# Performance work log

Hardware: AMD Instinct MI355X
Metric: run time of the kernel (lower is better)

## Reference

```python
import jax, jax.numpy as jnp
import numpy as np

B, S, HID = 2, 2048, 1024
NH, HD = 16, 64
EPS = 1e-12


def setup_inputs() -> dict:
    key = jax.random.key(0)
    ks = jax.random.split(key, 6)
    w_scale = 1.0 / np.sqrt(HID)
    return {
        "hidden_states": jax.random.normal(ks[0], (B, S, HID), dtype=jnp.float32),
        "attention_mask": jnp.ones((B, S), dtype=jnp.float32),
        "Wq": jax.random.normal(ks[1], (HID, HID), dtype=jnp.float32) * w_scale,
        "bq": jnp.zeros((HID,), dtype=jnp.float32),
        "Wk": jax.random.normal(ks[2], (HID, HID), dtype=jnp.float32) * w_scale,
        "bk": jnp.zeros((HID,), dtype=jnp.float32),
        "Wv": jax.random.normal(ks[3], (HID, HID), dtype=jnp.float32) * w_scale,
        "bv": jnp.zeros((HID,), dtype=jnp.float32),
        "Wd": jax.random.normal(ks[4], (HID, HID), dtype=jnp.float32) * w_scale,
        "bd": jnp.zeros((HID,), dtype=jnp.float32),
        "ln_gamma": jnp.ones((HID,), dtype=jnp.float32),
        "ln_beta": jnp.zeros((HID,), dtype=jnp.float32),
    }


def _heads(x):  # [B,S,HID] -> [B,NH,S,HD]
    return x.reshape(B, S, NH, HD).transpose(0, 2, 1, 3)


def reference(hidden_states, attention_mask, Wq, bq, Wk, bk, Wv, bv, Wd, bd, ln_gamma, ln_beta):
    # pre-LayerNorm
    mu = jnp.mean(hidden_states, axis=-1, keepdims=True)
    var = jnp.mean(jnp.square(hidden_states - mu), axis=-1, keepdims=True)
    h = (hidden_states - mu) * jax.lax.rsqrt(var + EPS) * ln_gamma + ln_beta

    q = _heads(h @ Wq.T + bq)  # [B,NH,S,HD]
    k = _heads(h @ Wk.T + bk)
    v = _heads(h @ Wv.T + bv)

    # additive mask: -1000 * (1 - mask), broadcast over heads and query pos
    add_mask = -1000.0 * (1.0 - attention_mask)[:, None, None, :]  # [B,1,1,S]

    # scale applied symmetrically to q and k: sqrt(sqrt(HD)) each
    scale = np.sqrt(np.sqrt(HD)).astype(np.float32)
    scores = jnp.einsum("bhqd,bhkd->bhqk", q / scale, k / scale) + add_mask
    probs = jax.nn.softmax(scores, axis=-1)  # dropout p=0 -> identity
    ctx = jnp.einsum("bhqk,bhkd->bhqd", probs, v)  # [B,NH,S,HD]

    ctx = ctx.transpose(0, 2, 1, 3).reshape(B, S, HID)
    return ctx @ Wd.T + bd
```

## Files before the change

kernel.cpp:

```cpp
#include <hip/hip_runtime.h>
#include <math.h>

#define BATCH 2
#define SEQ   2048
#define HID   1024
#define NH    16
#define HD    64
#define MROWS (BATCH * SEQ)
#define VSTR  4160

typedef unsigned short u16;
typedef short bf16x8 __attribute__((ext_vector_type(8)));
typedef float f32x4  __attribute__((ext_vector_type(4)));

#define LOG2E 1.4426950408889634f
#define C2    (0.125f * LOG2E)
#define M2F   23.083120f

static __device__ __forceinline__ u16 f2bf(float f) {
    union { float f; unsigned int u; } v; v.f = f;
    unsigned int r = (v.u + 0x7FFF + ((v.u >> 16) & 1)) >> 16;
    return (u16)r;
}

static __device__ __forceinline__ f32x4 mfma16(bf16x8 a, bf16x8 b, f32x4 c) {
    return __builtin_amdgcn_mfma_f32_16x16x32_bf16(a, b, c, 0, 0, 0);
}

static __device__ __forceinline__ void ldsload16(const void* g, void* l) {
    __builtin_amdgcn_global_load_lds(
        (const __attribute__((address_space(1))) void*)(unsigned long long)(uintptr_t)g,
        (__attribute__((address_space(3))) void*)(unsigned int)(uintptr_t)l,
        16, 0, 0);
}

__global__ __launch_bounds__(256) void prep_kernel(const float* __restrict__ x,
                                                   const float* __restrict__ gamma,
                                                   const float* __restrict__ beta,
                                                   u16* __restrict__ h,
                                                   const float* __restrict__ w0,
                                                   const float* __restrict__ w1,
                                                   const float* __restrict__ w2,
                                                   const float* __restrict__ w3,
                                                   u16* o0, u16* o1, u16* o2, u16* o3)
{
    __shared__ float red[8];
    const int t = threadIdx.x;
    if (blockIdx.x < 4096) {
        const int blk = blockIdx.x;
        const int which = blk >> 10;
        const int lb = blk & 1023;
        const float* src = which == 0 ? w0 : which == 1 ? w1 : which == 2 ? w2 : w3;
        u16* dst = which == 0 ? o0 : which == 1 ? o1 : which == 2 ? o2 : o3;
        const int idx = (lb * 256 + t) * 4;
        const float4 f = *(const float4*)(src + idx);
        union { u16 s[4]; uint2 v; } p;
        p.s[0] = f2bf(f.x); p.s[1] = f2bf(f.y); p.s[2] = f2bf(f.z); p.s[3] = f2bf(f.w);
        *(uint2*)(dst + idx) = p.v;
        return;
    }
    const int row = blockIdx.x - 4096;
    const float4 xv = ((const float4*)(x + (size_t)row * HID))[t];
    float s  = xv.x + xv.y + xv.z + xv.w;
    float ss = xv.x * xv.x + xv.y * xv.y + xv.z * xv.z + xv.w * xv.w;
#pragma unroll
    for (int off = 32; off > 0; off >>= 1) {
        s  += __shfl_down(s, off);
        ss += __shfl_down(ss, off);
    }
    const int wid = t >> 6;
    if ((t & 63) == 0) { red[wid] = s; red[4 + wid] = ss; }
    __syncthreads();
    s  = red[0] + red[1] + red[2] + red[3];
    ss = red[4] + red[5] + red[6] + red[7];
    const float mu   = s * (1.0f / HID);
    const float var  = ss * (1.0f / HID) - mu * mu;
    const float rstd = rsqrtf(var + 1e-12f);
    const float4 g  = ((const float4*)gamma)[t];
    const float4 bb = ((const float4*)beta)[t];
    union { u16 s[4]; uint2 v; } p;
    p.s[0] = f2bf((xv.x - mu) * rstd * g.x + bb.x);
    p.s[1] = f2bf((xv.y - mu) * rstd * g.y + bb.y);
    p.s[2] = f2bf((xv.z - mu) * rstd * g.z + bb.z);
    p.s[3] = f2bf((xv.w - mu) * rstd * g.w + bb.w);
    ((uint2*)(h + (size_t)row * HID))[t] = p.v;
}

static __device__ __forceinline__ void gemm_core(const u16* __restrict__ A,
                                                 const u16* __restrict__ B,
                                                 int K, int bm, int bn,
                                                 u16* As, u16* Bs,
                                                 int wave, int lane,
                                                 f32x4 acc[4][4])
{
    const int l15  = lane & 15;
    const int quad = lane >> 4;
    const int wm = (wave >> 1) * 64;
    const int wn = (wave & 1) * 64;

    const int c1 = wave * 64 + lane;
    const int c2 = c1 + 256;
    const u16* A1 = A + (size_t)(bm + (c1 >> 2)) * K + (c1 & 3) * 8;
    const u16* A2 = A + (size_t)(bm + (c2 >> 2)) * K + (c2 & 3) * 8;
    const u16* B1 = B + (size_t)(bn + (c1 >> 2)) * K + (c1 & 3) * 8;
    const u16* B2 = B + (size_t)(bn + (c2 >> 2)) * K + (c2 & 3) * 8;
    u16* lA1 = As + wave * 512;
    u16* lA2 = As + 2048 + wave * 512;
    u16* lB1 = Bs + wave * 512;
    u16* lB2 = Bs + 2048 + wave * 512;

    for (int k0 = 0; k0 < K; k0 += 32) {
        __syncthreads();
        ldsload16(A1 + k0, lA1);
        ldsload16(A2 + k0, lA2);
        ldsload16(B1 + k0, lB1);
        ldsload16(B2 + k0, lB2);
        __syncthreads();
        bf16x8 af[4], bfr[4];
#pragma unroll
        for (int mt = 0; mt < 4; mt++)
            af[mt] = *(const bf16x8*)&As[(wm + mt * 16 + l15) * 32 + quad * 8];
#pragma unroll
        for (int nt = 0; nt < 4; nt++)
            bfr[nt] = *(const bf16x8*)&Bs[(wn + nt * 16 + l15) * 32 + quad * 8];
#pragma unroll
        for (int mt = 0; mt < 4; mt++)
#pragma unroll
            for (int nt = 0; nt < 4; nt++)
                acc[mt][nt] = mfma16(af[mt], bfr[nt], acc[mt][nt]);
    }
}

__global__ __launch_bounds__(256) void qkv_gemm(const u16* __restrict__ h,
                                                const u16* __restrict__ wq,
                                                const u16* __restrict__ wk,
                                                const u16* __restrict__ wv,
                                                const float* __restrict__ bq,
                                                const float* __restrict__ bk,
                                                const float* __restrict__ bv,
                                                u16* __restrict__ qo,
                                                u16* __restrict__ ko,
                                                u16* __restrict__ vo)
{
    __shared__ u16 As[4096];
    __shared__ u16 Bs[4096];
    const int blk  = blockIdx.x;
    const int wave = threadIdx.x >> 6;
    const int lane = threadIdx.x & 63;
    const int l15  = lane & 15;
    const int quad = lane >> 4;
    const int wm = (wave >> 1) * 64;
    const int wn = (wave & 1) * 64;

    f32x4 acc[4][4];
#pragma unroll
    for (int mt = 0; mt < 4; mt++)
#pragma unroll
        for (int nt = 0; nt < 4; nt++) acc[mt][nt] = (f32x4)0.0f;

    if (blk < 512) {
        const u16* W     = (blk < 256) ? wq : wk;
        const float* bia = (blk < 256) ? bq : bk;
        u16* out         = (blk < 256) ? qo : ko;
        const int local = blk & 255;
        const int bm = (local >> 3) * 128;
        const int bn = (local & 7) * 128;
        gemm_core(h, W, HID, bm, bn, As, Bs, wave, lane, acc);

        float bv4[4];
#pragma unroll
        for (int nt = 0; nt < 4; nt++) bv4[nt] = bia[bn + wn + nt * 16 + l15];
#pragma unroll
        for (int mt = 0; mt < 4; mt++)
#pragma unroll
            for (int r = 0; r < 4; r++) {
                const int m  = bm + wm + mt * 16 + quad * 4 + r;
                const int bI = m >> 11;
                const int sI = m & (SEQ - 1);
#pragma unroll
                for (int nt = 0; nt < 4; nt++) {
                    const int n  = bn + wn + nt * 16 + l15;
                    const int hh = n >> 6;
                    const int d  = n & 63;
                    out[(((size_t)(bI * NH + hh) * SEQ + sI) << 6) + d] =
                        f2bf(acc[mt][nt][r] + bv4[nt]);
                }
            }
    } else {
        const int local = blk - 512;
        const int bm = (local & 7) * 128;
        const int bn = (local >> 3) * 128;
        gemm_core(wv, h, HID, bm, bn, As, Bs, wave, lane, acc);

#pragma unroll
        for (int mt = 0; mt < 4; mt++) {
            const f32x4 bm4 = *(const f32x4*)&bv[bm + wm + mt * 16 + quad * 4];
#pragma unroll
            for (int r = 0; r < 4; r++) {
                const int row = bm + wm + mt * 16 + quad * 4 + r;
#pragma unroll
                for (int nt = 0; nt < 4; nt++) {
                    const int col = bn + wn + nt * 16 + l15;
                    vo[(size_t)row * VSTR + col] = f2bf(acc[mt][nt][r] + bm4[r]);
                }
            }
        }
    }
}

__global__ __launch_bounds__(256) void out_gemm(const u16* __restrict__ ctx,
                                                const u16* __restrict__ wd,
                                                const float* __restrict__ bd,
                                                float* __restrict__ out)
{
    __shared__ u16 As[4096];
    __shared__ u16 Bs[4096];
    const int blk  = blockIdx.x;
    const int wave = threadIdx.x >> 6;
    const int lane = threadIdx.x & 63;
    const int l15  = lane & 15;
    const int quad = lane >> 4;
    const int wm = (wave >> 1) * 64;
    const int wn = (wave & 1) * 64;
    const int bm = (blk >> 3) * 128;
    const int bn = (blk & 7) * 128;

    f32x4 acc[4][4];
#pragma unroll
    for (int mt = 0; mt < 4; mt++)
#pragma unroll
        for (int nt = 0; nt < 4; nt++) acc[mt][nt] = (f32x4)0.0f;

    gemm_core(ctx, wd, HID, bm, bn, As, Bs, wave, lane, acc);

    float bv4[4];
#pragma unroll
    for (int nt = 0; nt < 4; nt++) bv4[nt] = bd[bn + wn + nt * 16 + l15];
#pragma unroll
    for (int mt = 0; mt < 4; mt++)
#pragma unroll
        for (int r = 0; r < 4; r++) {
            const int m = bm + wm + mt * 16 + quad * 4 + r;
#pragma unroll
            for (int nt = 0; nt < 4; nt++) {
                const int n = bn + wn + nt * 16 + l15;
                out[(size_t)m * HID + n] = acc[mt][nt][r] + bv4[nt];
            }
        }
}

__global__ __launch_bounds__(256) void attn_mfma(const u16* __restrict__ qb,
                                                 const u16* __restrict__ kb,
                                                 const u16* __restrict__ vtb,
                                                 const float* __restrict__ maskg,
                                                 u16* __restrict__ ctx)
{
    __shared__ __align__(16) char smem[25856];
    u16* Ks  = (u16*)smem;
    u16* Vts = (u16*)(smem + 8192);
    u16 (*Pw)[72] = (u16(*)[72])(smem + 16384 + (threadIdx.x >> 6) * 2304);
    float* Ms2 = (float*)(smem + 25600);

    const int t    = threadIdx.x;
    const int wave = t >> 6;
    const int lane = t & 63;
    const int l15  = lane & 15;
    const int quad = lane >> 4;

    const int bh = blockIdx.x & 31;
    const int qt = blockIdx.x >> 5;
    const int b  = bh >> 4;
    const int hh = bh & 15;
    const int q0 = qt * 64;

    const size_t headoff = (size_t)(b * NH + hh) * SEQ * HD;
    const u16* kbase = kb + headoff;
    const u16* vbase = vtb + (size_t)(hh * HD) * VSTR + b * SEQ;

    bf16x8 Qf[2];
    {
        const int qrow = q0 + wave * 16 + l15;
#pragma unroll
        for (int ks = 0; ks < 2; ks++)
            Qf[ks] = *(const bf16x8*)(qb + headoff + (size_t)qrow * HD + ks * 32 + quad * 8);
    }

    f32x4 O[4];
#pragma unroll
    for (int mt = 0; mt < 4; mt++) O[mt] = (f32x4)0.0f;
    float lsum = 0.0f;

    const int srow = lane >> 3;
    const int lcol = (lane & 7) ^ srow;
    const int sw0 = ((quad)     ^ (l15 & 7)) * 8;
    const int sw1 = ((quad + 4) ^ (l15 & 7)) * 8;

    for (int c0 = 0; c0 < SEQ; c0 += 64) {
        __syncthreads();
        {
            const int g0 = wave * 2;
            ldsload16(kbase + (size_t)(c0 + g0 * 8 + srow) * HD + lcol * 8,
                      (char*)Ks + g0 * 1024);
            ldsload16(kbase + (size_t)(c0 + g0 * 8 + 8 + srow) * HD + lcol * 8,
                      (char*)Ks + g0 * 1024 + 1024);
            ldsload16(vbase + (size_t)(g0 * 8 + srow) * VSTR + c0 + lcol * 8,
                      (char*)Vts + g0 * 1024);
            ldsload16(vbase + (size_t)(g0 * 8 + 8 + srow) * VSTR + c0 + lcol * 8,
                      (char*)Vts + g0 * 1024 + 1024);
            if (t < 64)
                Ms2[t] = fmaf(-1000.0f * (1.0f - maskg[b * SEQ + c0 + t]), LOG2E, -M2F);
        }
        __syncthreads();

        f32x4 St[4];
#pragma unroll
        for (int mt = 0; mt < 4; mt++) {
            const int rb = (mt * 16 + l15) * 64;
            const bf16x8 ka0 = *(const bf16x8*)&Ks[rb + sw0];
            const bf16x8 ka1 = *(const bf16x8*)&Ks[rb + sw1];
            f32x4 a = (f32x4)0.0f;
            a = mfma16(ka0, Qf[0], a);
            a = mfma16(ka1, Qf[1], a);
            St[mt] = a;
        }

#pragma unroll
        for (int mt = 0; mt < 4; mt++) {
            const f32x4 mv = *(const f32x4*)&Ms2[mt * 16 + quad * 4];
            union { u16 s[4]; uint2 v; } pk;
#pragma unroll
            for (int r = 0; r < 4; r++) {
                const float p = __builtin_amdgcn_exp2f(fmaf(St[mt][r], C2, mv[r]));
                lsum += p;
                pk.s[r] = f2bf(p);
            }
            *(uint2*)&Pw[l15][mt * 16 + quad * 4] = pk.v;
        }

        const bf16x8 Pb0 = *(const bf16x8*)&Pw[l15][quad * 8];
        const bf16x8 Pb1 = *(const bf16x8*)&Pw[l15][32 + quad * 8];

#pragma unroll
        for (int mt = 0; mt < 4; mt++) {
            const int rb = (mt * 16 + l15) * 64;
            const bf16x8 va0 = *(const bf16x8*)&Vts[rb + sw0];
            const bf16x8 va1 = *(const bf16x8*)&Vts[rb + sw1];
            O[mt] = mfma16(va0, Pb0, O[mt]);
            O[mt] = mfma16(va1, Pb1, O[mt]);
        }
    }

    lsum += __shfl_xor(lsum, 16);
    lsum += __shfl_xor(lsum, 32);
    const float linv = 1.0f / lsum;

    __syncthreads();
    float* Ot = (float*)smem + wave * (16 * 68);
#pragma unroll
    for (int mt = 0; mt < 4; mt++) {
        f32x4 v = O[mt] * linv;
        *(f32x4*)(Ot + l15 * 68 + mt * 16 + quad * 4) = v;
    }
    __syncthreads();
    {
        const int ql  = lane >> 2;
        const int seg = lane & 3;
        const float* srcp = Ot + ql * 68 + seg * 16;
        u16* dstp = ctx + (size_t)(b * SEQ + q0 + wave * 16 + ql) * HID
                        + hh * 64 + seg * 16;
#pragma unroll
        for (int j = 0; j < 2; j++) {
            union { u16 s[8]; uint4 v; } p;
#pragma unroll
            for (int i = 0; i < 8; i++) p.s[i] = f2bf(srcp[j * 8 + i]);
            *(uint4*)(dstp + j * 8) = p.v;
        }
    }
}

extern "C" void kernel_launch(void* const* d_in, const int* in_sizes, int n_in,
                              void* d_out, int out_size, void* d_ws, size_t ws_size,
                              hipStream_t stream)
{
    const float* hs    = (const float*)d_in[0];
    const float* mask  = (const float*)d_in[1];
    const float* Wq    = (const float*)d_in[2];
    const float* bq    = (const float*)d_in[3];
    const float* Wk    = (const float*)d_in[4];
    const float* bk    = (const float*)d_in[5];
    const float* Wv    = (const float*)d_in[6];
    const float* bv    = (const float*)d_in[7];
    const float* Wd    = (const float*)d_in[8];
    const float* bd    = (const float*)d_in[9];
    const float* gamma = (const float*)d_in[10];
    const float* beta  = (const float*)d_in[11];
    float* out = (float*)d_out;

    const size_t NE = (size_t)MROWS * HID;
    u16* ws   = (u16*)d_ws;
    u16* h    = ws;
    u16* qbb  = ws + NE;
    u16* kbb  = qbb + NE;
    u16* vtb  = kbb + NE;
    u16* ctxb = vtb + (size_t)HID * VSTR;
    u16* wqb  = ctxb + NE;
    u16* wkb  = wqb + HID * HID;
    u16* wvb  = wkb + HID * HID;
    u16* wdb  = wvb + HID * HID;

    prep_kernel<<<8192, 256, 0, stream>>>(hs, gamma, beta, h,
                                          Wq, Wk, Wv, Wd, wqb, wkb, wvb, wdb);

    qkv_gemm<<<768, 256, 0, stream>>>(h, wqb, wkb, wvb, bq, bk, bv, qbb, kbb, vtb);

    attn_mfma<<<1024, 256, 0, stream>>>(qbb, kbb, vtb, mask, ctxb);

    out_gemm<<<256, 256, 0, stream>>>(ctxb, wdb, bd, out);
}
```

Before: 236.8 us.

## Double-buffer LDS tiles in GEMMs and attention, precompute mask bias

The GEMM core and the attention loop now use double-buffered LDS tiles. The next K/V or A/B tile is issued with global_load_lds before computing on the current one, which drops one barrier per iteration. The additive mask term is computed once in extra blocks of the prep kernel into a workspace buffer, and attention reads it directly from global memory. P values are packed to bf16 with the paired hardware conversion. The cost is doubled LDS per block, which can lower occupancy, and extra workspace placed past the previous layout.

Measured after the change: 222.4 us. 6.1% less time.

```diff
diff --git a/kernel.cpp b/kernel.cpp
--- a/kernel.cpp
+++ b/kernel.cpp
@@ -1,4 +1,5 @@
 #include <hip/hip_runtime.h>
+#include <hip/hip_bf16.h>
 #include <math.h>
 
 #define BATCH 2
@@ -21,6 +22,13 @@
     union { float f; unsigned int u; } v; v.f = f;
     unsigned int r = (v.u + 0x7FFF + ((v.u >> 16) & 1)) >> 16;
     return (u16)r;
+}
+
+static __device__ __forceinline__ unsigned int pk_bf16(float a, float b) {
+    union { __hip_bfloat162 h; unsigned int u; } r;
+    float2 f; f.x = a; f.y = b;
+    r.h = __float22bfloat162_rn(f);
+    return r.u;
 }
 
 static __device__ __forceinline__ f32x4 mfma16(bf16x8 a, bf16x8 b, f32x4 c) {
@@ -42,10 +50,23 @@
                                                    const float* __restrict__ w1,
                                                    const float* __restrict__ w2,
                                                    const float* __restrict__ w3,
-                                                   u16* o0, u16* o1, u16* o2, u16* o3)
+                                                   u16* o0, u16* o1, u16* o2, u16* o3,
+                                                   const float* __restrict__ maskg,
+                                                   float* __restrict__ m2g)
 {
     __shared__ float red[8];
     const int t = threadIdx.x;
+    if (blockIdx.x >= 8192) {
+        const int idx = ((blockIdx.x - 8192) * 256 + t) * 4;
+        const float4 m = *(const float4*)(maskg + idx);
+        float4 o;
+        o.x = fmaf(-1000.0f * (1.0f - m.x), LOG2E, -M2F);
+        o.y = fmaf(-1000.0f * (1.0f - m.y), LOG2E, -M2F);
+        o.z = fmaf(-1000.0f * (1.0f - m.z), LOG2E, -M2F);
+        o.w = fmaf(-1000.0f * (1.0f - m.w), LOG2E, -M2F);
+        *(float4*)(m2g + idx) = o;
+        return;
+    }
     if (blockIdx.x < 4096) {
         const int blk = blockIdx.x;
         const int which = blk >> 10;
@@ -104,25 +125,33 @@
     const u16* A2 = A + (size_t)(bm + (c2 >> 2)) * K + (c2 & 3) * 8;
     const u16* B1 = B + (size_t)(bn + (c1 >> 2)) * K + (c1 & 3) * 8;
     const u16* B2 = B + (size_t)(bn + (c2 >> 2)) * K + (c2 & 3) * 8;
-    u16* lA1 = As + wave * 512;
-    u16* lA2 = As + 2048 + wave * 512;
-    u16* lB1 = Bs + wave * 512;
-    u16* lB2 = Bs + 2048 + wave * 512;
-
-    for (int k0 = 0; k0 < K; k0 += 32) {
+    const int o1 = wave * 512;
+    const int o2 = 2048 + wave * 512;
+
+    ldsload16(A1, As + o1);
+    ldsload16(A2, As + o2);
+    ldsload16(B1, Bs + o1);
+    ldsload16(B2, Bs + o2);
+
+    const int nstep = K >> 5;
+    for (int i = 0; i < nstep; i++) {
         __syncthreads();
-        ldsload16(A1 + k0, lA1);
-        ldsload16(A2 + k0, lA2);
-        ldsload16(B1 + k0, lB1);
-        ldsload16(B2 + k0, lB2);
-        __syncthreads();
+        const int cb = (i & 1) * 4096;
+        if (i + 1 < nstep) {
+            const int nb = ((i + 1) & 1) * 4096;
+            const int k0 = (i + 1) * 32;
+            ldsload16(A1 + k0, As + nb + o1);
+            ldsload16(A2 + k0, As + nb + o2);
+            ldsload16(B1 + k0, Bs + nb + o1);
+            ldsload16(B2 + k0, Bs + nb + o2);
+        }
         bf16x8 af[4], bfr[4];
 #pragma unroll
         for (int mt = 0; mt < 4; mt++)
-            af[mt] = *(const bf16x8*)&As[(wm + mt * 16 + l15) * 32 + quad * 8];
+            af[mt] = *(const bf16x8*)&As[cb + (wm + mt * 16 + l15) * 32 + quad * 8];
 #pragma unroll
         for (int nt = 0; nt < 4; nt++)
-            bfr[nt] = *(const bf16x8*)&Bs[(wn + nt * 16 + l15) * 32 + quad * 8];
+            bfr[nt] = *(const bf16x8*)&Bs[cb + (wn + nt * 16 + l15) * 32 + quad * 8];
 #pragma unroll
         for (int mt = 0; mt < 4; mt++)
 #pragma unroll
@@ -142,8 +171,8 @@
                                                 u16* __restrict__ ko,
                                                 u16* __restrict__ vo)
 {
-    __shared__ u16 As[4096];
-    __shared__ u16 Bs[4096];
+    __shared__ u16 As[8192];
+    __shared__ u16 Bs[8192];
     const int blk  = blockIdx.x;
     const int wave = threadIdx.x >> 6;
     const int lane = threadIdx.x & 63;
@@ -213,8 +242,8 @@
                                                 const float* __restrict__ bd,
                                                 float* __restrict__ out)
 {
-    __shared__ u16 As[4096];
-    __shared__ u16 Bs[4096];
+    __shared__ u16 As[8192];
+    __shared__ u16 Bs[8192];
     const int blk  = blockIdx.x;
     const int wave = threadIdx.x >> 6;
     const int lane = threadIdx.x & 63;
@@ -252,14 +281,11 @@
 __global__ __launch_bounds__(256) void attn_mfma(const u16* __restrict__ qb,
                                                  const u16* __restrict__ kb,
                                                  const u16* __restrict__ vtb,
-                                                 const float* __restrict__ maskg,
+                                                 const float* __restrict__ m2g,
                                                  u16* __restrict__ ctx)
 {
-    __shared__ __align__(16) char smem[25856];
-    u16* Ks  = (u16*)smem;
-    u16* Vts = (u16*)(smem + 8192);
-    u16 (*Pw)[72] = (u16(*)[72])(smem + 16384 + (threadIdx.x >> 6) * 2304);
-    float* Ms2 = (float*)(smem + 25600);
+    __shared__ __align__(16) char smem[41984];
+    u16 (*Pw)[72] = (u16(*)[72])(smem + 32768 + (threadIdx.x >> 6) * 2304);
 
     const int t    = threadIdx.x;
     const int wave = t >> 6;
@@ -276,6 +302,7 @@
     const size_t headoff = (size_t)(b * NH + hh) * SEQ * HD;
     const u16* kbase = kb + headoff;
     const u16* vbase = vtb + (size_t)(hh * HD) * VSTR + b * SEQ;
+    const float* m2b = m2g + b * SEQ;
 
     bf16x8 Qf[2];
     {
@@ -294,23 +321,27 @@
     const int lcol = (lane & 7) ^ srow;
     const int sw0 = ((quad)     ^ (l15 & 7)) * 8;
     const int sw1 = ((quad + 4) ^ (l15 & 7)) * 8;
-
-    for (int c0 = 0; c0 < SEQ; c0 += 64) {
+    const int g0 = wave * 2;
+
+    ldsload16(kbase + (size_t)(g0 * 8 + srow) * HD + lcol * 8,      smem + g0 * 1024);
+    ldsload16(kbase + (size_t)(g0 * 8 + 8 + srow) * HD + lcol * 8,  smem + g0 * 1024 + 1024);
+    ldsload16(vbase + (size_t)(g0 * 8 + srow) * VSTR + lcol * 8,    smem + 16384 + g0 * 1024);
+    ldsload16(vbase + (size_t)(g0 * 8 + 8 + srow) * VSTR + lcol * 8,smem + 16384 + g0 * 1024 + 1024);
+
+    for (int i = 0; i < 32; i++) {
         __syncthreads();
-        {
-            const int g0 = wave * 2;
-            ldsload16(kbase + (size_t)(c0 + g0 * 8 + srow) * HD + lcol * 8,
-                      (char*)Ks + g0 * 1024);
-            ldsload16(kbase + (size_t)(c0 + g0 * 8 + 8 + srow) * HD + lcol * 8,
-                      (char*)Ks + g0 * 1024 + 1024);
-            ldsload16(vbase + (size_t)(g0 * 8 + srow) * VSTR + c0 + lcol * 8,
-                      (char*)Vts + g0 * 1024);
-            ldsload16(vbase + (size_t)(g0 * 8 + 8 + srow) * VSTR + c0 + lcol * 8,
-                      (char*)Vts + g0 * 1024 + 1024);
-            if (t < 64)
-                Ms2[t] = fmaf(-1000.0f * (1.0f - maskg[b * SEQ + c0 + t]), LOG2E, -M2F);
-        }
-        __syncthreads();
+        const int c0 = i * 64;
+        const u16* Ks  = (const u16*)(smem + (i & 1) * 8192);
+        const u16* Vts = (const u16*)(smem + 16384 + (i & 1) * 8192);
+        if (i + 1 < 32) {
+            const int cn = c0 + 64;
+            char* nbK = smem + ((i + 1) & 1) * 8192;
+            char* nbV = smem + 16384 + ((i + 1) & 1) * 8192;
+            ldsload16(kbase + (size_t)(cn + g0 * 8 + srow) * HD + lcol * 8,      nbK + g0 * 1024);
+            ldsload16(kbase + (size_t)(cn + g0 * 8 + 8 + srow) * HD + lcol * 8,  nbK + g0 * 1024 + 1024);
+            ldsload16(vbase + (size_t)(g0 * 8 + srow) * VSTR + cn + lcol * 8,    nbV + g0 * 1024);
+            ldsload16(vbase + (size_t)(g0 * 8 + 8 + srow) * VSTR + cn + lcol * 8,nbV + g0 * 1024 + 1024);
+        }
 
         f32x4 St[4];
 #pragma unroll
@@ -326,15 +357,16 @@
 
 #pragma unroll
         for (int mt = 0; mt < 4; mt++) {
-            const f32x4 mv = *(const f32x4*)&Ms2[mt * 16 + quad * 4];
-            union { u16 s[4]; uint2 v; } pk;
-#pragma unroll
-            for (int r = 0; r < 4; r++) {
-                const float p = __builtin_amdgcn_exp2f(fmaf(St[mt][r], C2, mv[r]));
-                lsum += p;
-                pk.s[r] = f2bf(p);
-            }
-            *(uint2*)&Pw[l15][mt * 16 + quad * 4] = pk.v;
+            const f32x4 mv = *(const f32x4*)(m2b + c0 + mt * 16 + quad * 4);
+            float p0 = __builtin_amdgcn_exp2f(fmaf(St[mt][0], C2, mv[0]));
+            float p1 = __builtin_amdgcn_exp2f(fmaf(St[mt][1], C2, mv[1]));
+            float p2 = __builtin_amdgcn_exp2f(fmaf(St[mt][2], C2, mv[2]));
+            float p3 = __builtin_amdgcn_exp2f(fmaf(St[mt][3], C2, mv[3]));
+            lsum += p0 + p1 + p2 + p3;
+            uint2 w;
+            w.x = pk_bf16(p0, p1);
+            w.y = pk_bf16(p2, p3);
+            *(uint2*)&Pw[l15][mt * 16 + quad * 4] = w;
         }
 
         const bf16x8 Pb0 = *(const bf16x8*)&Pw[l15][quad * 8];
@@ -407,13 +439,15 @@
     u16* wkb  = wqb + HID * HID;
     u16* wvb  = wkb + HID * HID;
     u16* wdb  = wvb + HID * HID;
-
-    prep_kernel<<<8192, 256, 0, stream>>>(hs, gamma, beta, h,
-                                          Wq, Wk, Wv, Wd, wqb, wkb, wvb, wdb);
+    float* m2 = (float*)(wdb + HID * HID);
+
+    prep_kernel<<<8196, 256, 0, stream>>>(hs, gamma, beta, h,
+                                          Wq, Wk, Wv, Wd, wqb, wkb, wvb, wdb,
+                                          mask, m2);
 
     qkv_gemm<<<768, 256, 0, stream>>>(h, wqb, wkb, wvb, bq, bk, bv, qbb, kbb, vtb);
 
-    attn_mfma<<<1024, 256, 0, stream>>>(qbb, kbb, vtb, mask, ctxb);
+    attn_mfma<<<1024, 256, 0, stream>>>(qbb, kbb, vtb, m2, ctxb);
 
     out_gemm<<<256, 256, 0, stream>>>(ctxb, wdb, bd, out);
 }
```
